# Optimization experiments

Measured on AMD Instinct MI355X. Metric: run time of the kernel, lower is better.

The kernel has to match this reference:

```python
import math
import jax, jax.numpy as jnp
from jax import lax
import numpy as np

BSZ, NQ, L, DM, DI, H, HD, DDIST, DCONV, DHID = 2, 128, 2048, 256, 512, 8, 64, 16, 4, 64
DKEY = DI * 2 + 2 + H  # key_proj output: z + xbc + per-head dt bias
DCV = DI + 2           # depthwise conv channels


def setup_inputs() -> dict:
    key = jax.random.key(0)
    ks = jax.random.split(key, 40)
    it = iter(range(40))
    def n(shape, s=1.0):
        return jax.random.normal(ks[next(it)], shape, jnp.float32) * s
    # dt_bias init exactly as in torch module
    dt = jnp.exp(jax.random.uniform(ks[next(it)], (H,)) * (math.log(0.1) - math.log(0.001)) + math.log(0.001))
    dt = jnp.maximum(dt, 1e-4)
    dt_bias = dt + jnp.log(-jnp.expm1(-dt))
    A_log = jnp.log(jax.random.uniform(ks[next(it)], (H,), minval=1.0, maxval=16.0))
    return {
        'queries': n((BSZ, NQ, DM)), 'anchors': n((BSZ, NQ, 3), 10.0),
        'features_perm': n((BSZ, L, DM)), 'pos_embed_perm': n((BSZ, L, DM)),
        'key_pos_3d': n((BSZ, L, 3), 10.0), 'query_pos': n((BSZ, NQ, DM)),
        'key_proj_w': n((DM, DKEY), 0.02),
        'key_conv_w': n((DCV, DCONV), 0.1), 'key_conv_b': jnp.zeros((DCV,)),
        'query_proj_w': n((DM, DI), 0.02),
        'dist_w1': n((3, DHID), 0.3), 'dist_b1': jnp.zeros((DHID,)), 'dist_w2': n((DHID, DDIST), 0.1),
        'bc_proj_w': n((DDIST, 2), 0.2), 'dt_proj_w': n((DDIST, H), 0.2),
        'dt_bias': dt_bias, 'A_log': A_log, 'D': jnp.ones((H,)),
        'key_norm_w': jnp.ones((DI,)), 'out_key_proj_w': n((DI, DM), 0.02),
        'query_norm_w': jnp.ones((DI,)), 'query_norm_b': jnp.zeros((DI,)),
        'out_query_proj_w': n((DI, DM), 0.02),
        'ffn_norm_w': jnp.ones((DM,)), 'ffn_norm_b': jnp.zeros((DM,)),
        'ffn_fc1_w': n((DM, 8 * DM), 0.02), 'ffn_fc1_b': jnp.zeros((8 * DM,)),
        'ffn_fc2_w': n((4 * DM, DM), 0.02), 'ffn_fc2_b': jnp.zeros((DM,)),
    }


def _ln(x, w, b, eps=1e-5):
    m = jnp.mean(x, -1, keepdims=True)
    v = jnp.mean((x - m) ** 2, -1, keepdims=True)
    return (x - m) * lax.rsqrt(v + eps) * w + b


def _dwconv_causal(x, w, b):
    # x [B,L,C], w [C,K]; torch pads K-1 both sides then slices [:L] == causal left pad
    lhs = jnp.swapaxes(x, 1, 2)  # [B,C,L]
    out = lax.conv_general_dilated(lhs, w[:, None, :], (1,), [(DCONV - 1, 0)],
                                   feature_group_count=w.shape[0],
                                   dimension_numbers=('NCH', 'OIH', 'NCH'))
    return jnp.swapaxes(out + b[None, :, None], 1, 2)


def _issm(x, dt, A, Bs, Cs, Dp, init):
    # x [B,L,H,P]; dt [B,L,H,N]; A [H,N]; Bs/Cs [B,L,N]; init [B,H,P,N]
    def step(h, inp):
        xt, dtt, bt, ct = inp  # [B,H,P], [B,H,N], [B,N], [B,N]
        h = h * jnp.exp(dtt * A)[:, :, None, :] + (dtt * bt[:, None, :])[:, :, None, :] * xt[..., None]
        return h, jnp.einsum('bhpn,bn->bhp', h, ct)
    xs = (jnp.swapaxes(x, 0, 1), jnp.swapaxes(dt, 0, 1), jnp.swapaxes(Bs, 0, 1), jnp.swapaxes(Cs, 0, 1))
    h_last, ys = lax.scan(step, init, xs)
    y = jnp.swapaxes(ys, 0, 1) + x * Dp[None, None, :, None]  # D skip inside scan, as in ISSM_chunk_scan_combined
    return y, h_last


def _forward(queries, anchors, features_perm, pos_embed_perm, key_pos_3d, query_pos,
             key_proj_w, key_conv_w, key_conv_b, query_proj_w, dist_w1, dist_b1, dist_w2,
             bc_proj_w, dt_proj_w, dt_bias, A_log, D, key_norm_w, out_key_proj_w,
             query_norm_w, query_norm_b, out_query_proj_w, ffn_norm_w, ffn_norm_b,
             ffn_fc1_w, ffn_fc1_b, ffn_fc2_w, ffn_fc2_b):
    qp = queries + query_pos
    kp = (features_perm + pos_embed_perm) @ key_proj_w            # [B,L,DKEY]
    z, xbc, dtb_seq = kp[..., :DI], kp[..., DI:DI + DCV], kp[..., DI + DCV:]
    xbc = jax.nn.silu(_dwconv_causal(xbc, key_conv_w, key_conv_b))
    x = xbc[..., :DI]
    b_bias, c_bias = xbc[..., DI], xbc[..., DI + 1]               # [B,L]
    init = (qp @ query_proj_w).reshape(BSZ, NQ, H, HD).transpose(0, 2, 3, 1)  # [B,H,HD,NQ]
    # distance features: delta [B,L,NQ,3]
    delta = anchors[:, None, :, :] - key_pos_3d[:, :, None, :]
    enc = jnp.sign(delta) * jnp.log2(jnp.abs(delta) * 20.0 + 1.0) / math.log2(8.0) / 4.0
    feat = jax.nn.relu(enc @ dist_w1 + dist_b1) @ dist_w2         # [B,L,NQ,DDIST]
    bc = feat @ bc_proj_w                                         # [B,L,NQ,2]
    Bssm = bc[..., 0] + b_bias[..., None]                         # [B,L,NQ]
    Cssm = bc[..., 1] + c_bias[..., None]
    dtb = jnp.swapaxes(feat @ dt_proj_w, 2, 3)                    # [B,L,H,NQ]
    dt = jax.nn.softplus(dtb + dtb_seq[..., None] + dt_bias[None, None, :, None])
    A = jnp.broadcast_to(-jnp.exp(A_log)[:, None], (H, NQ))
    xs = x.reshape(BSZ, L, H, HD)
    y_f, h_f = _issm(xs, dt, A, Bssm, Cssm, D, init)
    fl = lambda a: jnp.flip(a, axis=1)
    y_b, h_b = _issm(fl(xs), fl(dt), A, fl(Bssm), fl(Cssm), D, init)
    y = (y_f + fl(y_b)) * 0.5
    h = (h_f + h_b) * 0.5                                         # [B,H,HD,NQ]
    y = y.reshape(BSZ, L, DI) + x * jnp.repeat(D, HD)[None, None, :]
    # gated RMSNorm (norm_before_gate=False): gate first, then normalize
    g = y * jax.nn.silu(z)
    g = g * lax.rsqrt(jnp.mean(g * g, -1, keepdims=True) + 1e-5) * key_norm_w
    out_feat = features_perm + g @ out_key_proj_w
    hs = h.transpose(0, 3, 1, 2).reshape(BSZ, NQ, DI)             # b h hd n -> b n (h hd)
    out_q = queries + _ln(hs, query_norm_w, query_norm_b) @ out_query_proj_w
    fn = _ln(out_q, ffn_norm_w, ffn_norm_b)
    a, v = jnp.split(fn @ ffn_fc1_w + ffn_fc1_b, 2, axis=-1)
    out_q = out_q + (jax.nn.gelu(a, approximate=False) * v) @ ffn_fc2_w + ffn_fc2_b
    return out_q, out_feat


def reference(queries, anchors, features_perm, pos_embed_perm, key_pos_3d, query_pos,
              key_proj_w, key_conv_w, key_conv_b, query_proj_w, dist_w1, dist_b1, dist_w2,
              bc_proj_w, dt_proj_w, dt_bias, A_log, D, key_norm_w, out_key_proj_w,
              query_norm_w, query_norm_b, out_query_proj_w, ffn_norm_w, ffn_norm_b,
              ffn_fc1_w, ffn_fc1_b, ffn_fc2_w, ffn_fc2_b):
    return _forward(queries, anchors, features_perm, pos_embed_perm, key_pos_3d, query_pos,
                    key_proj_w, key_conv_w, key_conv_b, query_proj_w, dist_w1, dist_b1, dist_w2,
                    bc_proj_w, dt_proj_w, dt_bias, A_log, D, key_norm_w, out_key_proj_w,
                    query_norm_w, query_norm_b, out_query_proj_w, ffn_norm_w, ffn_norm_b,
                    ffn_fc1_w, ffn_fc1_b, ffn_fc2_w, ffn_fc2_b)
```

## Files before the change

### kernel.cpp

```cpp
#include <hip/hip_runtime.h>

typedef unsigned short u16;
typedef __bf16 bf16x8 __attribute__((ext_vector_type(8)));
typedef u16 u16x8 __attribute__((ext_vector_type(8)));
typedef float f32x4 __attribute__((ext_vector_type(4)));
typedef float f32x2 __attribute__((ext_vector_type(2)));

#define BSZ_ 2
#define NQ_ 128
#define LSEQ_ 2048
#define DM_ 256
#define DI_ 512
#define NH_ 8
#define HD_ 64
#define DKEY_ 1034
#define DCV_ 514
#define NCHUNK_ 16
#define CT_ 128

__device__ __forceinline__ float bf2f(u16 u) {
  unsigned v = ((unsigned)u) << 16;
  return __builtin_bit_cast(float, v);
}
__device__ __forceinline__ u16 f2bf(float f) {
  unsigned u = __builtin_bit_cast(unsigned, f);
  u += 0x7fffu + ((u >> 16) & 1u);
  return (u16)(u >> 16);
}
__device__ __forceinline__ float sigmoidf_(float x) { return 1.f / (1.f + expf(-x)); }
__device__ __forceinline__ float softplusf_(float x) {
  return (x > 20.f) ? x : log1pf(expf(x));
}

template<bool F32>
__device__ __forceinline__ float ldi(const void* p, size_t i) {
  return F32 ? ((const float*)p)[i] : bf2f(((const u16*)p)[i]);
}
template<bool F32>
__device__ __forceinline__ void sto(void* p, size_t i, float v) {
  if (F32) ((float*)p)[i] = v;
  else ((u16*)p)[i] = f2bf(v);
}

__device__ __forceinline__ bool detect_f32(const void* feat) {
  int lane = threadIdx.x & 63;
  float a = fabsf(bf2f(((const u16*)feat)[2*lane]));
  bool plaus = (a > 1e-6f) && (a < 1e6f);
  unsigned long long m = __ballot(plaus);
  return __popcll(m) < 32;
}

constexpr size_t SZ_KP    = (size_t)BSZ_*LSEQ_*DKEY_;
constexpr size_t SZ_XACT  = (size_t)BSZ_*LSEQ_*DCV_;
constexpr size_t SZ_AW    = (size_t)BSZ_*NH_*LSEQ_*NQ_*2;
constexpr size_t SZ_CARR  = (size_t)BSZ_*LSEQ_*NQ_;
constexpr size_t SZ_QPROJ = (size_t)BSZ_*NQ_*DI_;
constexpr size_t SZ_YACC  = (size_t)BSZ_*LSEQ_*DI_;
constexpr size_t SZ_SEND  = (size_t)BSZ_*NH_*2*NCHUNK_*NQ_*HD_;
constexpr size_t SZ_PTOT  = (size_t)BSZ_*NH_*2*NCHUNK_*NQ_;
constexpr size_t SZ_H0    = SZ_SEND;
constexpr size_t SZ_HB    = (size_t)BSZ_*NH_*2*NQ_*HD_;
constexpr size_t SZ_GBUF  = (size_t)BSZ_*LSEQ_*DI_/2;
constexpr size_t SZ_OUTQF = (size_t)BSZ_*NQ_*DM_;
constexpr size_t SZ_WPREP = 2048;

constexpr size_t OFF_KP    = 0;
constexpr size_t OFF_XACT  = OFF_KP + SZ_KP;
constexpr size_t OFF_AW    = OFF_XACT + SZ_XACT;
constexpr size_t OFF_CARR  = OFF_AW + SZ_AW;
constexpr size_t OFF_QPROJ = OFF_CARR + SZ_CARR;
constexpr size_t OFF_YACC  = OFF_QPROJ + SZ_QPROJ;
constexpr size_t OFF_SEND  = OFF_YACC + SZ_YACC;
constexpr size_t OFF_PTOT  = OFF_SEND + SZ_SEND;
constexpr size_t OFF_H0    = OFF_PTOT + SZ_PTOT;
constexpr size_t OFF_HB    = OFF_H0 + SZ_H0;
constexpr size_t OFF_GBUF  = OFF_HB + SZ_HB;
constexpr size_t OFF_OUTQF = OFF_GBUF + SZ_GBUF;
constexpr size_t OFF_WPREP = OFF_OUTQF + SZ_OUTQF;
constexpr size_t WS_FLOATS = OFF_WPREP + SZ_WPREP;

constexpr size_t OFF_UG  = OFF_AW;
constexpr size_t OFF_LNQ = OFF_UG + (size_t)256*1024/2;
constexpr size_t OFF_LNF = OFF_LNQ + (size_t)256*512/2;

constexpr size_t OFF_ABUF = OFF_SEND;
constexpr size_t OFF_AQ   = OFF_ABUF + (size_t)4096*256/2;
constexpr size_t OFF_BKEY = OFF_AQ + (size_t)256*256/2;
constexpr size_t OFF_BQ   = OFF_BKEY + (size_t)(256*1034+1)/2 + 1;
constexpr size_t OFF_BOK  = OFF_SEND;
constexpr size_t OFF_BOQ  = OFF_BOK + (size_t)512*256/2;
constexpr size_t OFF_B1W  = OFF_BOQ + (size_t)512*256/2;
constexpr size_t OFF_B2W  = OFF_B1W + (size_t)256*2048/2;

template<bool F32>
__device__ void prep_body(const void* A_log, const void* dt_bias,
                          const void* w1, const void* b1, const void* w2,
                          const void* bcw, const void* dtw, float* wp) {
  int t = threadIdx.x;
  if (t < 8) {
    wp[t]     = -expf(ldi<F32>(A_log, t));
    wp[8 + t] = ldi<F32>(dt_bias, t);
  }
  if (t < 64) {
    wp[32 + t*4 + 0] = ldi<F32>(w1, 0*64 + t);
    wp[32 + t*4 + 1] = ldi<F32>(w1, 1*64 + t);
    wp[32 + t*4 + 2] = ldi<F32>(w1, 2*64 + t);
    wp[32 + t*4 + 3] = ldi<F32>(b1, t);
  }
  for (int i = t; i < 1024; i += 256) wp[288 + i] = ldi<F32>(w2, i);
  if (t < 32)  wp[1312 + t] = ldi<F32>(bcw, t);
  if (t < 128) wp[1344 + t] = ldi<F32>(dtw, t);
}

__device__ __forceinline__ void cast_job(bool F32, const void* s0, const void* s1_,
                                         u16* d, size_t n, size_t base, size_t stride) {
  for (size_t i = base; i < n; i += stride) {
    float v = F32 ? ((const float*)s0)[i] : bf2f(((const u16*)s0)[i]);
    if (s1_) v += F32 ? ((const float*)s1_)[i] : bf2f(((const u16*)s1_)[i]);
    d[i] = f2bf(v);
  }
}

__global__ __launch_bounds__(256) void setup_kernel(
    const void* feat, const void* pe, u16* abuf,
    const void* q, const void* qp, u16* aq,
    const void* kw, u16* bkey, const void* qw, u16* bq,
    const void* A_log, const void* dt_bias, const void* w1, const void* b1,
    const void* w2, const void* bcw, const void* dtw, float* wp,
    float* yacc, int* flag)
{
  int bx = blockIdx.x, tid = threadIdx.x;
  if (bx < 512) {
    size_t base = (size_t)bx * 4096 + tid;
#pragma unroll
    for (int k = 0; k < 16; ++k) yacc[base + (size_t)k*256] = 0.f;
    return;
  }
  bool F32 = detect_f32(feat);
  if (bx < 1024) {
    cast_job(F32, feat, pe, abuf, (size_t)4096*256,
             (size_t)(bx-512)*256 + tid, (size_t)512*256);
  } else if (bx < 1056) {
    cast_job(F32, q, qp, aq, (size_t)256*256,
             (size_t)(bx-1024)*256 + tid, (size_t)32*256);
  } else if (bx < 1184) {
    cast_job(F32, kw, nullptr, bkey, (size_t)256*1034,
             (size_t)(bx-1056)*256 + tid, (size_t)128*256);
  } else if (bx < 1248) {
    cast_job(F32, qw, nullptr, bq, (size_t)256*512,
             (size_t)(bx-1184)*256 + tid, (size_t)64*256);
  } else {
    if (tid == 0) *flag = F32 ? 1 : 0;
    if (F32) prep_body<true>(A_log, dt_bias, w1, b1, w2, bcw, dtw, wp);
    else     prep_body<false>(A_log, dt_bias, w1, b1, w2, bcw, dtw, wp);
  }
}

template<int A_MODE, int B_MODE, int OUT_EXT, int RES_EXT, int RES_F32, int BIAS, bool F32>
__device__ void gemm_body(int bm, int bn,
                          const void* A0, const void* A1, const void* Bw,
                          float* Cf, void* Cext, const void* ResE,
                          const float* ResF, const void* Bias,
                          int M, int N, int K) {
  __shared__ u16 As[64][40];
  __shared__ u16 Bs[64][42];
  int tid = threadIdx.x;
  int w = tid >> 6, lane = tid & 63;
  f32x4 acc[4];
#pragma unroll
  for (int j = 0; j < 4; ++j) acc[j] = (f32x4){0.f, 0.f, 0.f, 0.f};

  int arow = tid >> 2, aseg = (tid & 3) * 8;
  int bkl = tid >> 3, bns = (tid & 7) * 8;

  for (int k0 = 0; k0 < K; k0 += 32) {
    {
      size_t abase = (size_t)(bm + arow) * K + k0 + aseg;
      u16x8 tv;
      if (A_MODE == 0) {
#pragma unroll
        for (int i = 0; i < 8; ++i)
          tv[i] = f2bf(ldi<F32>(A0, abase + i) + ldi<F32>(A1, abase + i));
      } else {
        const u16* pa = (const u16*)A0 + abase;
#pragma unroll
        for (int i = 0; i < 8; ++i) tv[i] = pa[i];
      }
      *(u16x8*)&As[arow][aseg] = tv;
    }
    {
      size_t bbase = (size_t)(k0 + bkl) * N + bn + bns;
#pragma unroll
      for (int i = 0; i < 8; ++i) {
        u16 v;
        if (bn + bns + i < N) {
          if (B_MODE == 1) v = ((const u16*)Bw)[bbase + i];
          else             v = f2bf(ldi<F32>(Bw, bbase + i));
        } else v = (u16)0;
        Bs[bns + i][bkl] = v;
      }
    }
    __syncthreads();
    int mrow = w * 16 + (lane & 15);
    int kq = (lane >> 4) * 8;
    bf16x8 af = __builtin_bit_cast(bf16x8, *(const u16x8*)&As[mrow][kq]);
#pragma unroll
    for (int j = 0; j < 4; ++j) {
      bf16x8 bfv = __builtin_bit_cast(bf16x8, *(const u16x8*)&Bs[j*16 + (lane & 15)][kq]);
      acc[j] = __builtin_amdgcn_mfma_f32_16x16x32_bf16(af, bfv, acc[j], 0, 0, 0);
    }
    __syncthreads();
  }
  int col0 = lane & 15, rbase = (lane >> 4) * 4;
#pragma unroll
  for (int j = 0; j < 4; ++j) {
#pragma unroll
    for (int r = 0; r < 4; ++r) {
      int row = bm + w * 16 + rbase + r;
      int col = bn + j * 16 + col0;
      if (col < N) {
        size_t idx = (size_t)row * N + col;
        float v = acc[j][r];
        if (BIAS)    v += ldi<F32>(Bias, col);
        if (RES_EXT) v += ldi<F32>(ResE, idx);
        if (RES_F32) v += ResF[idx];
        if (OUT_EXT) sto<F32>(Cext, idx, v);
        else         Cf[idx] = v;
      }
    }
  }
}

__global__ __launch_bounds__(256) void kp_gemm_kernel(
    const u16* abuf, const u16* bkey, float* kp) {
  gemm_body<1,1,0,0,0,0,false>(blockIdx.x*64, blockIdx.y*64, abuf, nullptr, bkey,
                               kp, nullptr, nullptr, nullptr, nullptr,
                               4096, DKEY_, DM_);
}

template<bool F32>
__device__ void fc2_body(const u16* ug, const u16* b2w, void* out_q,
                         const float* outqf, const void* b2) {
  gemm_body<1,1,1,0,1,1,F32>((blockIdx.x&3)*64, (blockIdx.x>>2)*64, ug, nullptr,
                             b2w, nullptr, out_q, nullptr, outqf, b2,
                             BSZ_*NQ_, DM_, 1024);
}
__global__ __launch_bounds__(256) void fc2_kernel(
    const int* fl, const u16* ug, const u16* b2w, void* out_q,
    const float* outqf, const void* b2) {
  if (*fl) fc2_body<true>(ug, b2w, out_q, outqf, b2);
  else     fc2_body<false>(ug, b2w, out_q, outqf, b2);
}

template<bool F32>
__device__ void conv_body(const float* kp, const void* cw, const void* cb,
                          float* xact) {
  int row = blockIdx.x;
  int l = row & (LSEQ_ - 1);
  for (int ch = threadIdx.x; ch < DCV_; ch += 256) {
    float acc = ldi<F32>(cb, ch);
#pragma unroll
    for (int k = 0; k < 4; ++k) {
      int ll = l - 3 + k;
      if (ll >= 0)
        acc = fmaf(ldi<F32>(cw, ch*4 + k), kp[(size_t)(row - 3 + k)*DKEY_ + DI_ + ch], acc);
    }
    xact[(size_t)row*DCV_ + ch] = acc * sigmoidf_(acc);
  }
}
__global__ __launch_bounds__(256) void convqp_kernel(
    const int* fl, const float* kp, const void* cw, const void* cb, float* xact,
    const u16* aq, const u16* bq, float* qproj)
{
  int bx = blockIdx.x;
  if (bx < 4096) {
    if (*fl) conv_body<true>(kp, cw, cb, xact);
    else     conv_body<false>(kp, cw, cb, xact);
  } else {
    int i = bx - 4096;
    gemm_body<1,1,0,0,0,0,false>((i&3)*64, (i>>2)*64, aq, nullptr, bq,
                                 qproj, nullptr, nullptr, nullptr, nullptr,
                                 BSZ_*NQ_, DI_, DM_);
  }
}

template<bool F32>
__device__ void dist_body(const void* anchors, const void* key_pos,
                          const float* kp, const float* xact, const float* wp,
                          float* aw, float* carr) {
  int tid = threadIdx.x;
  int n = tid & 127;
  int idx = blockIdx.x;
  int b = idx >> 10;
  int l = ((idx & 1023) << 1) | (tid >> 7);
  size_t row = (size_t)b * LSEQ_ + l;

  float enc0, enc1, enc2;
  {
    float e[3];
#pragma unroll
    for (int d = 0; d < 3; ++d) {
      float delta = ldi<F32>(anchors, (b*NQ_ + n)*3 + d) - ldi<F32>(key_pos, row*3 + d);
      float s = delta < 0.f ? -1.f : 1.f;
      e[d] = s * log2f(fabsf(delta) * 20.f + 1.f) * (1.f/12.f);
    }
    enc0 = e[0]; enc1 = e[1]; enc2 = e[2];
  }
  float feat[16];
#pragma unroll
  for (int f = 0; f < 16; ++f) feat[f] = 0.f;
  for (int j = 0; j < 64; ++j) {
    float w0 = wp[32 + j*4], w1v = wp[33 + j*4], w2v = wp[34 + j*4], bb = wp[35 + j*4];
    float hj = fmaxf(fmaf(enc0, w0, fmaf(enc1, w1v, fmaf(enc2, w2v, bb))), 0.f);
#pragma unroll
    for (int f = 0; f < 16; ++f) feat[f] = fmaf(hj, wp[288 + j*16 + f], feat[f]);
  }
  float bc0 = 0.f, bc1 = 0.f;
#pragma unroll
  for (int f = 0; f < 16; ++f) {
    bc0 = fmaf(feat[f], wp[1312 + f*2], bc0);
    bc1 = fmaf(feat[f], wp[1313 + f*2], bc1);
  }
  float bb_ = xact[row*DCV_ + DI_];
  float cb_ = xact[row*DCV_ + DI_ + 1];
  float Bs = bc0 + bb_, Cs = bc1 + cb_;
  carr[row*NQ_ + n] = Cs;

  float dtb[8];
#pragma unroll
  for (int h = 0; h < 8; ++h) dtb[h] = 0.f;
#pragma unroll
  for (int f = 0; f < 16; ++f)
#pragma unroll
    for (int h = 0; h < 8; ++h) dtb[h] = fmaf(feat[f], wp[1344 + f*8 + h], dtb[h]);

#pragma unroll
  for (int h = 0; h < 8; ++h) {
    float xln = dtb[h] + kp[row*DKEY_ + (DI_*2 + 2) + h] + wp[8 + h];
    float dtv = softplusf_(xln);
    float a = expf(dtv * wp[h]);
    float wv = dtv * Bs;
    size_t o = (((size_t)(b*NH_ + h)*LSEQ_ + l)*NQ_ + n)*2;
    aw[o] = a;
    aw[o + 1] = wv;
  }
}
__global__ __launch_bounds__(256) void dist_kernel(
    const int* fl, const void* anchors, const void* key_pos, const float* kp,
    const float* xact, const float* wp, float* aw, float* carr) {
  if (*fl) dist_body<true>(anchors, key_pos, kp, xact, wp, aw, carr);
  else     dist_body<false>(anchors, key_pos, kp, xact, wp, aw, carr);
}

__global__ __launch_bounds__(256) void s1m_kernel(
    const float* __restrict__ aw, const float* __restrict__ xact,
    float* __restrict__ send, float* __restrict__ ptot)
{
  __shared__ float awl[2][8][32];
  __shared__ float xl [2][8][64];
  int tid = threadIdx.x;
  int hd = tid & 63;
  int w = __builtin_amdgcn_readfirstlane(tid >> 6);
  int ns = blockIdx.x, q = blockIdx.y, z = blockIdx.z;
  int h = z & 7, b = z >> 3;
  int n0 = __builtin_amdgcn_readfirstlane(ns*16 + w*4);

  float hf[4], hb[4], pr[4];
#pragma unroll
  for (int i = 0; i < 4; ++i) { hf[i] = 0.f; hb[i] = 0.f; pr[i] = 1.f; }

  int s8 = tid >> 5, j = tid & 31;
  int t0 = q*CT_;
  const float* awg = aw + (size_t)z*LSEQ_*(NQ_*2)
                     + (size_t)(t0 + s8)*(NQ_*2) + ns*32 + j;
  const float* xg  = xact + ((size_t)(b*LSEQ_) + t0 + s8)*DCV_ + (h<<6) + j*2;
  const long awgstep = 8L*(NQ_*2);
  const long xgstep  = 8L*DCV_;

  {
    float pa = *awg;
    f32x2 px = *(const f32x2*)xg;
    awg += awgstep; xg += xgstep;
    awl[0][s8][j] = pa;
    *(f32x2*)&xl[0][s8][j*2] = px;
  }
  asm volatile("s_waitcnt lgkmcnt(0)" ::: "memory");
  __builtin_amdgcn_s_barrier();

  int p = 0;
  float sa; f32x2 sx;
  for (int g = 0; g < 16; ++g) {
    if (g < 15) {
      sa = *awg; sx = *(const f32x2*)xg;
      awg += awgstep; xg += xgstep;
    }
#pragma unroll
    for (int s = 0; s < 8; ++s) {
      const float* A = &awl[p][s][w*8];
      float xv = xl[p][s][hd];
#pragma unroll
      for (int i = 0; i < 4; ++i) {
        float a = A[2*i], wv = A[2*i + 1];
        float wx = wv * xv;
        hf[i] = fmaf(hf[i], a, wx);
        hb[i] = fmaf(pr[i], wx, hb[i]);
        pr[i] *= a;
      }
    }
    if (g < 15) {
      awl[p^1][s8][j] = sa;
      *(f32x2*)&xl[p^1][s8][j*2] = sx;
    }
    asm volatile("s_waitcnt lgkmcnt(0)" ::: "memory");
    __builtin_amdgcn_s_barrier();
    p ^= 1;
  }

  size_t cbf = (size_t)((z*2 + 0)*NCHUNK_ + q);
  size_t cbb = (size_t)((z*2 + 1)*NCHUNK_ + (NCHUNK_ - 1 - q));
#pragma unroll
  for (int i = 0; i < 4; ++i) {
    send[cbf*(NQ_*HD_) + (size_t)(n0 + i)*HD_ + hd] = hf[i];
    send[cbb*(NQ_*HD_) + (size_t)(n0 + i)*HD_ + hd] = hb[i];
  }
  if (hd == 0) {
#pragma unroll
    for (int i = 0; i < 4; ++i) {
      ptot[cbf*NQ_ + n0 + i] = pr[i];
      ptot[cbb*NQ_ + n0 + i] = pr[i];
    }
  }
}

__global__ __launch_bounds__(256) void s2_kernel(
    const float* __restrict__ qproj, const float* __restrict__ ptot,
    const float* __restrict__ send, float* __restrict__ h0buf,
    float* __restrict__ hbuf)
{
  int g = blockIdx.x*256 + threadIdx.x;
  int hd = g & 63;
  int n = (g >> 6) & 127;
  int dir = (g >> 13) & 1;
  int h = (g >> 14) & 7;
  int b = g >> 17;
  float hcur = qproj[((size_t)(b*NQ_ + n))*DI_ + h*HD_ + hd];
  size_t base = (size_t)((b*NH_ + h)*2 + dir) * NCHUNK_;
  for (int q = 0; q < NCHUNK_; ++q) {
    size_t cb = base + q;
    h0buf[cb*(NQ_*HD_) + (size_t)n*HD_ + hd] = hcur;
    hcur = fmaf(hcur, ptot[cb*NQ_ + n], send[cb*(NQ_*HD_) + (size_t)n*HD_ + hd]);
  }
  hbuf[((size_t)((b*NH_ + h)*2 + dir))*(NQ_*HD_) + (size_t)n*HD_ + hd] = hcur;
}

template<bool F32>
__device__ void cast1_part(const void* okw, u16* bok, const void* oqw, u16* boq,
                           const void* w1, u16* b1w, const void* w2, u16* b2w) {
  int i = blockIdx.x - 2048;
  int job = i >> 7, bj = i & 127;
  size_t base = (size_t)bj*256 + threadIdx.x, stride = (size_t)128*256;
  switch (job) {
    case 0: cast_job(F32, okw, nullptr, bok, (size_t)512*256, base, stride); break;
    case 1: cast_job(F32, oqw, nullptr, boq, (size_t)512*256, base, stride); break;
    case 2: cast_job(F32, w1, nullptr, b1w, (size_t)256*2048, base, stride); break;
    default: cast_job(F32, w2, nullptr, b2w, (size_t)1024*256, base, stride); break;
  }
}
__global__ __launch_bounds__(256) void s3cast_kernel(
    const int* fl, const float* __restrict__ aw, const float* __restrict__ carr,
    const float* __restrict__ xact, const float* __restrict__ h0buf,
    float* __restrict__ yacc,
    const void* okw, u16* bok, const void* oqw, u16* boq,
    const void* w1, u16* b1w, const void* w2, u16* b2w)
{
  int bx = blockIdx.x;
  if (bx >= 2048) {
    if (*fl) cast1_part<true>(okw, bok, oqw, boq, w1, b1w, w2, b2w);
    else     cast1_part<false>(okw, bok, oqw, boq, w1, b1w, w2, b2w);
    return;
  }
  __shared__ float awl[2][8][64];
  __shared__ float ctl[2][8][32];
  __shared__ float xl [2][8][64];
  __shared__ float yl [8][4][64];

  int tid = threadIdx.x;
  int hd = tid & 63;
  int w = __builtin_amdgcn_readfirstlane(tid >> 6);
  int ns = bx & 3, q = (bx >> 2) & 15, zz = bx >> 6;
  int dir = zz & 1, h = (zz >> 1) & 7, b = zz >> 4;
  int z = b*NH_ + h;
  int n0 = ns*32 + w*8;

  int tbase = dir ? (LSEQ_ - 1 - q*CT_) : (q*CT_);
  int tstep = dir ? -1 : 1;

  int s8 = tid >> 5, j = tid & 31;
  const float* awg = aw + (size_t)z*LSEQ_*(NQ_*2)
                     + (size_t)(tbase + tstep*s8)*(NQ_*2) + ns*64 + j*2;
  const float* ctg = carr + ((size_t)(b*LSEQ_) + tbase + tstep*s8)*NQ_ + ns*32 + j;
  const float* xg  = xact + ((size_t)(b*LSEQ_) + tbase + tstep*s8)*DCV_ + (h<<6) + j*2;
  long awgstep = (long)tstep*8*(NQ_*2);
  long ctgstep = (long)tstep*8*NQ_;
  long xgstep  = (long)tstep*8*DCV_;

  f32x2 pa = *(const f32x2*)awg;
  float pc = *ctg;
  f32x2 px = *(const f32x2*)xg;
  awg += awgstep; ctg += ctgstep; xg += xgstep;

  float h0_, h1_, h2_, h3_, h4_, h5_, h6_, h7_;
  {
    size_t cb = (size_t)((z*2 + dir)*NCHUNK_ + q);
    const float* hp = h0buf + cb*(NQ_*HD_) + (size_t)n0*HD_ + hd;
    h0_ = hp[0*HD_]; h1_ = hp[1*HD_]; h2_ = hp[2*HD_]; h3_ = hp[3*HD_];
    h4_ = hp[4*HD_]; h5_ = hp[5*HD_]; h6_ = hp[6*HD_]; h7_ = hp[7*HD_];
  }
  *(f32x2*)&awl[0][s8][j*2] = pa;
  ctl[0][s8][j] = pc;
  *(f32x2*)&xl[0][s8][j*2] = px;
  asm volatile("s_waitcnt lgkmcnt(0)" ::: "memory");
  __builtin_amdgcn_s_barrier();

  float* yrow = yacc + ((size_t)(b*LSEQ_) + tbase)*DI_ + (h << 6) + hd;
  long ystep = (long)tstep * DI_;

  int p = 0;
  f32x2 sa; float sc; f32x2 sx;
  for (int g = 0; g < 16; ++g) {
    if (g < 15) {
      sa = *(const f32x2*)awg; sc = *ctg; sx = *(const f32x2*)xg;
      awg += awgstep; ctg += ctgstep; xg += xgstep;
    }
    if (g > 0) {
#pragma unroll
      for (int r = 0; r < 2; ++r) {
        int s = w + r*4;
        float yv = yl[s][0][hd] + yl[s][1][hd] + yl[s][2][hd] + yl[s][3][hd];
        atomicAdd(yrow + (long)((g-1)*8 + s)*ystep, 0.5f * yv);
      }
    }
    asm volatile("s_waitcnt lgkmcnt(0)" ::: "memory");
    __builtin_amdgcn_s_barrier();
#pragma unroll
    for (int s = 0; s < 8; ++s) {
      const float* A = &awl[p][s][w*16];
      const float* C = &ctl[p][s][w*8];
      float xv = xl[p][s][hd];
      float ya, yb;
      h0_ = fmaf(h0_, A[0],  A[1]*xv);  ya = h0_ * C[0];
      h1_ = fmaf(h1_, A[2],  A[3]*xv);  yb = h1_ * C[1];
      h2_ = fmaf(h2_, A[4],  A[5]*xv);  ya = fmaf(h2_, C[2], ya);
      h3_ = fmaf(h3_, A[6],  A[7]*xv);  yb = fmaf(h3_, C[3], yb);
      h4_ = fmaf(h4_, A[8],  A[9]*xv);  ya = fmaf(h4_, C[4], ya);
      h5_ = fmaf(h5_, A[10], A[11]*xv); yb = fmaf(h5_, C[5], yb);
      h6_ = fmaf(h6_, A[12], A[13]*xv); ya = fmaf(h6_, C[6], ya);
      h7_ = fmaf(h7_, A[14], A[15]*xv); yb = fmaf(h7_, C[7], yb);
      yl[s][w][hd] = ya + yb;
    }
    if (g < 15) {
      *(f32x2*)&awl[p^1][s8][j*2] = sa;
      ctl[p^1][s8][j] = sc;
      *(f32x2*)&xl[p^1][s8][j*2] = sx;
    }
    asm volatile("s_waitcnt lgkmcnt(0)" ::: "memory");
    __builtin_amdgcn_s_barrier();
    p ^= 1;
  }
#pragma unroll
  for (int r = 0; r < 2; ++r) {
    int s = w + r*4;
    float yv = yl[s][0][hd] + yl[s][1][hd] + yl[s][2][hd] + yl[s][3][hd];
    atomicAdd(yrow + (long)(15*8 + s)*ystep, 0.5f * yv);
  }
}

__device__ __forceinline__ float block_sum256(float v, float* red) {
#pragma unroll
  for (int off = 32; off; off >>= 1) v += __shfl_xor(v, off, 64);
  int wv = threadIdx.x >> 6;
  if ((threadIdx.x & 63) == 0) red[wv] = v;
  __syncthreads();
  float t = red[0] + red[1] + red[2] + red[3];
  __syncthreads();
  return t;
}

template<bool F32>
__device__ void g_body(const float* yacc, const float* xact, const float* kp,
                       const void* Dv, const void* knw, u16* gbuf) {
  int row = blockIdx.x, tid = threadIdx.x;
  __shared__ float red[4];
  float gg[2];
  float ss = 0.f;
#pragma unroll
  for (int ii = 0; ii < 2; ++ii) {
    int ch = tid + ii*256;
    float yv = yacc[(size_t)row*DI_ + ch];
    float xv = xact[(size_t)row*DCV_ + ch];
    float zv = kp[(size_t)row*DKEY_ + ch];
    float Dh = ldi<F32>(Dv, ch >> 6);
    float yf = yv + 2.f * Dh * xv;
    float g = yf * (zv * sigmoidf_(zv));
    gg[ii] = g;
    ss += g * g;
  }
  float tot = block_sum256(ss, red);
  float r = rsqrtf(tot / (float)DI_ + 1e-5f);
#pragma unroll
  for (int ii = 0; ii < 2; ++ii) {
    int ch = tid + ii*256;
    gbuf[(size_t)row*DI_ + ch] = f2bf(gg[ii] * r * ldi<F32>(knw, ch));
  }
}
template<bool F32>
__device__ void lnq_body(const float* hbuf, const void* qnw, const void* qnb,
                         u16* lnq) {
  int row = blockIdx.x - 4096;
  int b = row >> 7, n = row & 127;
  int tid = threadIdx.x;
  __shared__ float red[4];
  float hv[2];
  float s1 = 0.f, s2 = 0.f;
#pragma unroll
  for (int ii = 0; ii < 2; ++ii) {
    int ch = tid + ii*256;
    int h = ch >> 6, hd = ch & 63;
    size_t base = ((size_t)((b*NH_ + h)*2))*(NQ_*HD_) + (size_t)n*HD_ + hd;
    float v = 0.5f * (hbuf[base] + hbuf[base + (size_t)NQ_*HD_]);
    hv[ii] = v;
    s1 += v;
    s2 += v * v;
  }
  s1 = block_sum256(s1, red);
  s2 = block_sum256(s2, red);
  float mean = s1 / (float)DI_;
  float var = fmaxf(s2 / (float)DI_ - mean * mean, 0.f);
  float rstd = rsqrtf(var + 1e-5f);
#pragma unroll
  for (int ii = 0; ii < 2; ++ii) {
    int ch = tid + ii*256;
    lnq[(size_t)row*DI_ + ch] =
        f2bf((hv[ii] - mean) * rstd * ldi<F32>(qnw, ch) + ldi<F32>(qnb, ch));
  }
}
__global__ __launch_bounds__(256) void glnq_kernel(
    const int* fl, const float* yacc, const float* xact, const float* kp,
    const void* Dv, const void* knw, u16* gbuf,
    const float* hbuf, const void* qnw, const void* qnb, u16* lnq)
{
  if (blockIdx.x < 4096) {
    if (*fl) g_body<true>(yacc, xact, kp, Dv, knw, gbuf);
    else     g_body<false>(yacc, xact, kp, Dv, knw, gbuf);
  } else {
    if (*fl) lnq_body<true>(hbuf, qnw, qnb, lnq);
    else     lnq_body<false>(hbuf, qnw, qnb, lnq);
  }
}

template<bool F32>
__device__ void ofoq_body(const u16* gbuf, const u16* bok, void* out_feat,
                          const void* features, const u16* lnq, const u16* boq,
                          float* outqf, const void* queries) {
  int bx = blockIdx.x;
  if (bx < 256) {
    gemm_body<1,1,1,1,0,0,F32>((bx>>2)*64, (bx&3)*64, gbuf, nullptr, bok,
                               nullptr, out_feat, features, nullptr, nullptr,
                               4096, DM_, DI_);
  } else {
    int i = bx - 256;
    gemm_body<1,1,0,1,0,0,F32>((i&3)*64, (i>>2)*64, lnq, nullptr, boq,
                               outqf, nullptr, queries, nullptr, nullptr,
                               BSZ_*NQ_, DM_, DI_);
  }
}
__global__ __launch_bounds__(256) void ofoq_kernel(
    const int* fl, const u16* gbuf, const u16* bok,
    void* out_feat_f32, void* out_feat_bf16, const void* features,
    const u16* lnq, const u16* boq, float* outqf, const void* queries) {
  if (*fl) ofoq_body<true>(gbuf, bok, out_feat_f32, features, lnq, boq, outqf, queries);
  else     ofoq_body<false>(gbuf, bok, out_feat_bf16, features, lnq, boq, outqf, queries);
}

template<bool F32>
__device__ void lnf_body(const float* outqf, const void* fnw, const void* fnb,
                         u16* lnf) {
  int row = blockIdx.x, tid = threadIdx.x;
  __shared__ float red[4];
  float x = outqf[(size_t)row*DM_ + tid];
  float s1 = block_sum256(x, red);
  float s2 = block_sum256(x * x, red);
  float mean = s1 / (float)DM_;
  float var = fmaxf(s2 / (float)DM_ - mean * mean, 0.f);
  float rstd = rsqrtf(var + 1e-5f);
  lnf[(size_t)row*DM_ + tid] =
      f2bf((x - mean) * rstd * ldi<F32>(fnw, tid) + ldi<F32>(fnb, tid));
}
__global__ __launch_bounds__(256) void lnf_kernel(
    const int* fl, const float* outqf, const void* fnw, const void* fnb, u16* lnf) {
  if (*fl) lnf_body<true>(outqf, fnw, fnb, lnf);
  else     lnf_body<false>(outqf, fnw, fnb, lnf);
}

template<bool F32>
__device__ void fc1g_body(const u16* lnf, const u16* b1w, const void* b1, u16* ug) {
  __shared__ u16 As[64][40];
  __shared__ u16 BsA[64][42];
  __shared__ u16 BsV[64][42];
  int tid = threadIdx.x;
  int w = tid >> 6, lane = tid & 63;
  int bm = blockIdx.x * 64, bn = blockIdx.y * 64;
  f32x4 accA[4], accV[4];
#pragma unroll
  for (int j = 0; j < 4; ++j) {
    accA[j] = (f32x4){0.f, 0.f, 0.f, 0.f};
    accV[j] = (f32x4){0.f, 0.f, 0.f, 0.f};
  }
  int arow = tid >> 2, aseg = (tid & 3) * 8;
  int bkl = tid >> 3, bns = (tid & 7) * 8;

  for (int k0 = 0; k0 < DM_; k0 += 32) {
    {
      size_t abase = (size_t)(bm + arow) * DM_ + k0 + aseg;
      const u16* pa = lnf + abase;
      u16x8 tv;
#pragma unroll
      for (int i = 0; i < 8; ++i) tv[i] = pa[i];
      *(u16x8*)&As[arow][aseg] = tv;
    }
    {
      size_t bbase = (size_t)(k0 + bkl) * 2048 + bn + bns;
#pragma unroll
      for (int i = 0; i < 8; ++i) {
        BsA[bns + i][bkl] = b1w[bbase + i];
        BsV[bns + i][bkl] = b1w[bbase + 1024 + i];
      }
    }
    __syncthreads();
    int mrow = w * 16 + (lane & 15);
    int kq = (lane >> 4) * 8;
    bf16x8 af = __builtin_bit_cast(bf16x8, *(const u16x8*)&As[mrow][kq]);
#pragma unroll
    for (int j = 0; j < 4; ++j) {
      bf16x8 ba = __builtin_bit_cast(bf16x8, *(const u16x8*)&BsA[j*16 + (lane & 15)][kq]);
      bf16x8 bv = __builtin_bit_cast(bf16x8, *(const u16x8*)&BsV[j*16 + (lane & 15)][kq]);
      accA[j] = __builtin_amdgcn_mfma_f32_16x16x32_bf16(af, ba, accA[j], 0, 0, 0);
      accV[j] = __builtin_amdgcn_mfma_f32_16x16x32_bf16(af, bv, accV[j], 0, 0, 0);
    }
    __syncthreads();
  }
  int col0 = lane & 15, rbase = (lane >> 4) * 4;
#pragma unroll
  for (int j = 0; j < 4; ++j) {
#pragma unroll
    for (int r = 0; r < 4; ++r) {
      int row = bm + w * 16 + rbase + r;
      int col = bn + j * 16 + col0;
      float a = accA[j][r] + ldi<F32>(b1, col);
      float v = accV[j][r] + ldi<F32>(b1, col + 1024);
      float ge = 0.5f * a * (1.f + erff(a * 0.70710678118f));
      ug[(size_t)row*1024 + col] = f2bf(ge * v);
    }
  }
}
__global__ __launch_bounds__(256) void fc1g_kernel(
    const int* fl, const u16* lnf, const u16* b1w, const void* b1, u16* ug) {
  if (*fl) fc1g_body<true>(lnf, b1w, b1, ug);
  else     fc1g_body<false>(lnf, b1w, b1, ug);
}

extern "C" void kernel_launch(void* const* d_in, const int* in_sizes, int n_in,
                              void* d_out, int out_size, void* d_ws, size_t ws_size,
                              hipStream_t stream) {
  const void* queries        = d_in[0];
  const void* anchors        = d_in[1];
  const void* features       = d_in[2];
  const void* pos_embed      = d_in[3];
  const void* key_pos        = d_in[4];
  const void* query_pos      = d_in[5];
  const void* key_proj_w     = d_in[6];
  const void* key_conv_w     = d_in[7];
  const void* key_conv_b     = d_in[8];
  const void* query_proj_w   = d_in[9];
  const void* dist_w1        = d_in[10];
  const void* dist_b1        = d_in[11];
  const void* dist_w2        = d_in[12];
  const void* bc_proj_w      = d_in[13];
  const void* dt_proj_w      = d_in[14];
  const void* dt_bias        = d_in[15];
  const void* A_log          = d_in[16];
  const void* Dvec           = d_in[17];
  const void* key_norm_w     = d_in[18];
  const void* out_key_proj_w = d_in[19];
  const void* query_norm_w   = d_in[20];
  const void* query_norm_b   = d_in[21];
  const void* out_query_proj_w = d_in[22];
  const void* ffn_norm_w     = d_in[23];
  const void* ffn_norm_b     = d_in[24];
  const void* ffn_fc1_w      = d_in[25];
  const void* ffn_fc1_b      = d_in[26];
  const void* ffn_fc2_w      = d_in[27];
  const void* ffn_fc2_b      = d_in[28];

  if (ws_size < WS_FLOATS * sizeof(float)) return;

  float* ws    = (float*)d_ws;
  float* kp    = ws + OFF_KP;
  float* xact  = ws + OFF_XACT;
  float* aw    = ws + OFF_AW;
  float* carr  = ws + OFF_CARR;
  float* qproj = ws + OFF_QPROJ;
  float* yacc  = ws + OFF_YACC;
  float* send  = ws + OFF_SEND;
  float* ptot  = ws + OFF_PTOT;
  float* h0buf = ws + OFF_H0;
  float* hbuf  = ws + OFF_HB;
  u16*   gbuf  = (u16*)(ws + OFF_GBUF);
  float* outqf = ws + OFF_OUTQF;
  float* wprep = ws + OFF_WPREP;
  int*   flag  = (int*)(wprep + 1536);
  u16*   ugbuf = (u16*)(ws + OFF_UG);
  u16*   lnq   = (u16*)(ws + OFF_LNQ);
  u16*   lnf   = (u16*)(ws + OFF_LNF);
  u16*   abuf  = (u16*)(ws + OFF_ABUF);
  u16*   aq    = (u16*)(ws + OFF_AQ);
  u16*   bkey  = (u16*)(ws + OFF_BKEY);
  u16*   bq    = (u16*)(ws + OFF_BQ);
  u16*   bok   = (u16*)(ws + OFF_BOK);
  u16*   boq   = (u16*)(ws + OFF_BOQ);
  u16*   b1w   = (u16*)(ws + OFF_B1W);
  u16*   b2w   = (u16*)(ws + OFF_B2W);

  void* out_q = d_out;
  void* out_feat_bf16 = (void*)((u16*)d_out + (size_t)BSZ_*NQ_*DM_);
  void* out_feat_f32  = (void*)((float*)d_out + (size_t)BSZ_*NQ_*DM_);

  setup_kernel<<<1249, 256, 0, stream>>>(
      features, pos_embed, abuf, queries, query_pos, aq,
      key_proj_w, bkey, query_proj_w, bq,
      A_log, dt_bias, dist_w1, dist_b1, dist_w2, bc_proj_w, dt_proj_w, wprep,
      yacc, flag);

  kp_gemm_kernel<<<dim3(64, 17), 256, 0, stream>>>(abuf, bkey, kp);

  convqp_kernel<<<4096 + 32, 256, 0, stream>>>(
      flag, kp, key_conv_w, key_conv_b, xact, aq, bq, qproj);

  dist_kernel<<<BSZ_*LSEQ_/2, 256, 0, stream>>>(flag, anchors, key_pos, kp, xact,
                                                wprep, aw, carr);

  s1m_kernel<<<dim3(8, NCHUNK_, BSZ_*NH_), 256, 0, stream>>>(aw, xact, send, ptot);

  s2_kernel<<<1024, 256, 0, stream>>>(qproj, ptot, send, h0buf, hbuf);

  s3cast_kernel<<<2048 + 512, 256, 0, stream>>>(
      flag, aw, carr, xact, h0buf, yacc,
      out_key_proj_w, bok, out_query_proj_w, boq, ffn_fc1_w, b1w, ffn_fc2_w, b2w);

  glnq_kernel<<<4096 + 256, 256, 0, stream>>>(
      flag, yacc, xact, kp, Dvec, key_norm_w, gbuf,
      hbuf, query_norm_w, query_norm_b, lnq);

  ofoq_kernel<<<256 + 16, 256, 0, stream>>>(
      flag, gbuf, bok, out_feat_f32, out_feat_bf16, features,
      lnq, boq, outqf, queries);

  lnf_kernel<<<BSZ_*NQ_, 256, 0, stream>>>(flag, outqf, ffn_norm_w, ffn_norm_b, lnf);

  fc1g_kernel<<<dim3(4, 16), 256, 0, stream>>>(flag, lnf, b1w, ffn_fc1_b, ugbuf);

  fc2_kernel<<<16, 256, 0, stream>>>(flag, ugbuf, b2w, out_q, outqf, ffn_fc2_b);
}
```

Measured before the change: 423.0 us.

## Fuse conv/dist/qproj launches, fold FFN LayerNorm into fc1, vectorize GEMM loads

New measurement: 437.8 us. +3.5%, slower.

```diff
diff --git a/kernel.cpp b/kernel.cpp
--- a/kernel.cpp
+++ b/kernel.cpp
@@ -3,6 +3,7 @@
 typedef unsigned short u16;
 typedef __bf16 bf16x8 __attribute__((ext_vector_type(8)));
 typedef u16 u16x8 __attribute__((ext_vector_type(8)));
+typedef u16 u16x2 __attribute__((ext_vector_type(2)));
 typedef float f32x4 __attribute__((ext_vector_type(4)));
 typedef float f32x2 __attribute__((ext_vector_type(2)));
 
@@ -81,7 +82,6 @@
 
 constexpr size_t OFF_UG  = OFF_AW;
 constexpr size_t OFF_LNQ = OFF_UG + (size_t)256*1024/2;
-constexpr size_t OFF_LNF = OFF_LNQ + (size_t)256*512/2;
 
 constexpr size_t OFF_ABUF = OFF_SEND;
 constexpr size_t OFF_AQ   = OFF_ABUF + (size_t)4096*256/2;
@@ -156,7 +156,7 @@
   }
 }
 
-template<int A_MODE, int B_MODE, int OUT_EXT, int RES_EXT, int RES_F32, int BIAS, bool F32>
+template<int A_MODE, int B_MODE, int BV, int OUT_EXT, int RES_EXT, int RES_F32, int BIAS, bool F32>
 __device__ void gemm_body(int bm, int bn,
                           const void* A0, const void* A1, const void* Bw,
                           float* Cf, void* Cext, const void* ResE,
@@ -182,22 +182,34 @@
         for (int i = 0; i < 8; ++i)
           tv[i] = f2bf(ldi<F32>(A0, abase + i) + ldi<F32>(A1, abase + i));
       } else {
-        const u16* pa = (const u16*)A0 + abase;
-#pragma unroll
-        for (int i = 0; i < 8; ++i) tv[i] = pa[i];
+        tv = *(const u16x8*)((const u16*)A0 + abase);
       }
       *(u16x8*)&As[arow][aseg] = tv;
     }
     {
       size_t bbase = (size_t)(k0 + bkl) * N + bn + bns;
-#pragma unroll
-      for (int i = 0; i < 8; ++i) {
-        u16 v;
-        if (bn + bns + i < N) {
-          if (B_MODE == 1) v = ((const u16*)Bw)[bbase + i];
-          else             v = f2bf(ldi<F32>(Bw, bbase + i));
-        } else v = (u16)0;
-        Bs[bns + i][bkl] = v;
+      if (BV == 2) {
+        u16x8 bv8 = *(const u16x8*)((const u16*)Bw + bbase);
+#pragma unroll
+        for (int i = 0; i < 8; ++i) Bs[bns + i][bkl] = bv8[i];
+      } else if (BV == 1 && bn + bns + 8 <= N) {
+        const u16* bp = (const u16*)Bw + bbase;
+#pragma unroll
+        for (int i2 = 0; i2 < 4; ++i2) {
+          u16x2 v2 = *(const u16x2*)(bp + i2*2);
+          Bs[bns + i2*2][bkl]     = v2[0];
+          Bs[bns + i2*2 + 1][bkl] = v2[1];
+        }
+      } else {
+#pragma unroll
+        for (int i = 0; i < 8; ++i) {
+          u16 v;
+          if (bn + bns + i < N) {
+            if (B_MODE == 1) v = ((const u16*)Bw)[bbase + i];
+            else             v = f2bf(ldi<F32>(Bw, bbase + i));
+          } else v = (u16)0;
+          Bs[bns + i][bkl] = v;
+        }
       }
     }
     __syncthreads();
@@ -233,17 +245,17 @@
 
 __global__ __launch_bounds__(256) void kp_gemm_kernel(
     const u16* abuf, const u16* bkey, float* kp) {
-  gemm_body<1,1,0,0,0,0,false>(blockIdx.x*64, blockIdx.y*64, abuf, nullptr, bkey,
-                               kp, nullptr, nullptr, nullptr, nullptr,
-                               4096, DKEY_, DM_);
+  gemm_body<1,1,1,0,0,0,0,false>(blockIdx.x*64, blockIdx.y*64, abuf, nullptr, bkey,
+                                 kp, nullptr, nullptr, nullptr, nullptr,
+                                 4096, DKEY_, DM_);
 }
 
 template<bool F32>
 __device__ void fc2_body(const u16* ug, const u16* b2w, void* out_q,
                          const float* outqf, const void* b2) {
-  gemm_body<1,1,1,0,1,1,F32>((blockIdx.x&3)*64, (blockIdx.x>>2)*64, ug, nullptr,
-                             b2w, nullptr, out_q, nullptr, outqf, b2,
-                             BSZ_*NQ_, DM_, 1024);
+  gemm_body<1,1,2,1,0,1,1,F32>((blockIdx.x&3)*64, (blockIdx.x>>2)*64, ug, nullptr,
+                               b2w, nullptr, out_q, nullptr, outqf, b2,
+                               BSZ_*NQ_, DM_, 1024);
 }
 __global__ __launch_bounds__(256) void fc2_kernel(
     const int* fl, const u16* ug, const u16* b2w, void* out_q,
@@ -254,8 +266,7 @@
 
 template<bool F32>
 __device__ void conv_body(const float* kp, const void* cw, const void* cb,
-                          float* xact) {
-  int row = blockIdx.x;
+                          float* xact, int row) {
   int l = row & (LSEQ_ - 1);
   for (int ch = threadIdx.x; ch < DCV_; ch += 256) {
     float acc = ldi<F32>(cb, ch);
@@ -268,26 +279,11 @@
     xact[(size_t)row*DCV_ + ch] = acc * sigmoidf_(acc);
   }
 }
-__global__ __launch_bounds__(256) void convqp_kernel(
-    const int* fl, const float* kp, const void* cw, const void* cb, float* xact,
-    const u16* aq, const u16* bq, float* qproj)
-{
-  int bx = blockIdx.x;
-  if (bx < 4096) {
-    if (*fl) conv_body<true>(kp, cw, cb, xact);
-    else     conv_body<false>(kp, cw, cb, xact);
-  } else {
-    int i = bx - 4096;
-    gemm_body<1,1,0,0,0,0,false>((i&3)*64, (i>>2)*64, aq, nullptr, bq,
-                                 qproj, nullptr, nullptr, nullptr, nullptr,
-                                 BSZ_*NQ_, DI_, DM_);
-  }
-}
 
 template<bool F32>
 __device__ void dist_body(const void* anchors, const void* key_pos,
-                          const float* kp, const float* xact, const float* wp,
-                          float* aw, float* carr) {
+                          const float* kp, const void* cw, const void* cb,
+                          const float* wp, float* aw, float* carr) {
   int tid = threadIdx.x;
   int n = tid & 127;
   int idx = blockIdx.x;
@@ -306,6 +302,19 @@
     }
     enc0 = e[0]; enc1 = e[1]; enc2 = e[2];
   }
+  float acc0 = ldi<F32>(cb, 512);
+  float acc1 = ldi<F32>(cb, 513);
+#pragma unroll
+  for (int k = 0; k < 4; ++k) {
+    int ll = l - 3 + k;
+    if (ll >= 0) {
+      acc0 = fmaf(ldi<F32>(cw, 512*4 + k), kp[(row - 3 + k)*DKEY_ + DI_ + 512], acc0);
+      acc1 = fmaf(ldi<F32>(cw, 513*4 + k), kp[(row - 3 + k)*DKEY_ + DI_ + 513], acc1);
+    }
+  }
+  float bb_ = acc0 * sigmoidf_(acc0);
+  float cb_ = acc1 * sigmoidf_(acc1);
+
   float feat[16];
 #pragma unroll
   for (int f = 0; f < 16; ++f) feat[f] = 0.f;
@@ -321,8 +330,6 @@
     bc0 = fmaf(feat[f], wp[1312 + f*2], bc0);
     bc1 = fmaf(feat[f], wp[1313 + f*2], bc1);
   }
-  float bb_ = xact[row*DCV_ + DI_];
-  float cb_ = xact[row*DCV_ + DI_ + 1];
   float Bs = bc0 + bb_, Cs = bc1 + cb_;
   carr[row*NQ_ + n] = Cs;
 
@@ -345,11 +352,26 @@
     aw[o + 1] = wv;
   }
 }
-__global__ __launch_bounds__(256) void dist_kernel(
-    const int* fl, const void* anchors, const void* key_pos, const float* kp,
-    const float* xact, const float* wp, float* aw, float* carr) {
-  if (*fl) dist_body<true>(anchors, key_pos, kp, xact, wp, aw, carr);
-  else     dist_body<false>(anchors, key_pos, kp, xact, wp, aw, carr);
+
+__global__ __launch_bounds__(256) void cdq_kernel(
+    const int* fl, const float* kp, const void* cw, const void* cb, float* xact,
+    const u16* aq, const u16* bq, float* qproj,
+    const void* anchors, const void* key_pos, const float* wp,
+    float* aw, float* carr)
+{
+  int bx = blockIdx.x;
+  if (bx < 2048) {
+    if (*fl) dist_body<true>(anchors, key_pos, kp, cw, cb, wp, aw, carr);
+    else     dist_body<false>(anchors, key_pos, kp, cw, cb, wp, aw, carr);
+  } else if (bx < 6144) {
+    if (*fl) conv_body<true>(kp, cw, cb, xact, bx - 2048);
+    else     conv_body<false>(kp, cw, cb, xact, bx - 2048);
+  } else {
+    int i = bx - 6144;
+    gemm_body<1,1,2,0,0,0,0,false>((i&3)*64, (i>>2)*64, aq, nullptr, bq,
+                                   qproj, nullptr, nullptr, nullptr, nullptr,
+                                   BSZ_*NQ_, DI_, DM_);
+  }
 }
 
 __global__ __launch_bounds__(256) void s1m_kernel(
@@ -664,14 +686,14 @@
                           float* outqf, const void* queries) {
   int bx = blockIdx.x;
   if (bx < 256) {
-    gemm_body<1,1,1,1,0,0,F32>((bx>>2)*64, (bx&3)*64, gbuf, nullptr, bok,
-                               nullptr, out_feat, features, nullptr, nullptr,
-                               4096, DM_, DI_);
+    gemm_body<1,1,2,1,1,0,0,F32>((bx>>2)*64, (bx&3)*64, gbuf, nullptr, bok,
+                                 nullptr, out_feat, features, nullptr, nullptr,
+                                 4096, DM_, DI_);
   } else {
     int i = bx - 256;
-    gemm_body<1,1,0,1,0,0,F32>((i&3)*64, (i>>2)*64, lnq, nullptr, boq,
-                               outqf, nullptr, queries, nullptr, nullptr,
-                               BSZ_*NQ_, DM_, DI_);
+    gemm_body<1,1,2,0,1,0,0,F32>((i&3)*64, (i>>2)*64, lnq, nullptr, boq,
+                                 outqf, nullptr, queries, nullptr, nullptr,
+                                 BSZ_*NQ_, DM_, DI_);
   }
 }
 __global__ __launch_bounds__(256) void ofoq_kernel(
@@ -683,63 +705,63 @@
 }
 
 template<bool F32>
-__device__ void lnf_body(const float* outqf, const void* fnw, const void* fnb,
-                         u16* lnf) {
-  int row = blockIdx.x, tid = threadIdx.x;
-  __shared__ float red[4];
-  float x = outqf[(size_t)row*DM_ + tid];
-  float s1 = block_sum256(x, red);
-  float s2 = block_sum256(x * x, red);
-  float mean = s1 / (float)DM_;
-  float var = fmaxf(s2 / (float)DM_ - mean * mean, 0.f);
-  float rstd = rsqrtf(var + 1e-5f);
-  lnf[(size_t)row*DM_ + tid] =
-      f2bf((x - mean) * rstd * ldi<F32>(fnw, tid) + ldi<F32>(fnb, tid));
-}
-__global__ __launch_bounds__(256) void lnf_kernel(
-    const int* fl, const float* outqf, const void* fnw, const void* fnb, u16* lnf) {
-  if (*fl) lnf_body<true>(outqf, fnw, fnb, lnf);
-  else     lnf_body<false>(outqf, fnw, fnb, lnf);
-}
-
-template<bool F32>
-__device__ void fc1g_body(const u16* lnf, const u16* b1w, const void* b1, u16* ug) {
-  __shared__ u16 As[64][40];
+__device__ void fc1g_body(const float* outqf, const void* fnw, const void* fnb,
+                          const u16* b1w, const void* b1, u16* ug) {
+  __shared__ u16 Asf[64][264];
   __shared__ u16 BsA[64][42];
   __shared__ u16 BsV[64][42];
+  __shared__ float red1[64][4];
+  __shared__ float red2[64][4];
   int tid = threadIdx.x;
   int w = tid >> 6, lane = tid & 63;
   int bm = blockIdx.x * 64, bn = blockIdx.y * 64;
+
+  {
+    int r = tid >> 2, qt = tid & 3;
+    const float* src = outqf + (size_t)(bm + r)*DM_ + qt*64;
+    float v[64];
+    float s1 = 0.f, s2 = 0.f;
+#pragma unroll
+    for (int i = 0; i < 64; ++i) { v[i] = src[i]; s1 += v[i]; s2 += v[i]*v[i]; }
+    red1[r][qt] = s1; red2[r][qt] = s2;
+    __syncthreads();
+    float t1 = red1[r][0] + red1[r][1] + red1[r][2] + red1[r][3];
+    float t2 = red2[r][0] + red2[r][1] + red2[r][2] + red2[r][3];
+    float mean = t1 / (float)DM_;
+    float var = fmaxf(t2 / (float)DM_ - mean * mean, 0.f);
+    float rstd = rsqrtf(var + 1e-5f);
+#pragma unroll
+    for (int i = 0; i < 64; ++i) {
+      int col = qt*64 + i;
+      Asf[r][col] = f2bf((v[i] - mean) * rstd * ldi<F32>(fnw, col)
+                         + ldi<F32>(fnb, col));
+    }
+    __syncthreads();
+  }
+
   f32x4 accA[4], accV[4];
 #pragma unroll
   for (int j = 0; j < 4; ++j) {
     accA[j] = (f32x4){0.f, 0.f, 0.f, 0.f};
     accV[j] = (f32x4){0.f, 0.f, 0.f, 0.f};
   }
-  int arow = tid >> 2, aseg = (tid & 3) * 8;
   int bkl = tid >> 3, bns = (tid & 7) * 8;
 
   for (int k0 = 0; k0 < DM_; k0 += 32) {
     {
-      size_t abase = (size_t)(bm + arow) * DM_ + k0 + aseg;
-      const u16* pa = lnf + abase;
-      u16x8 tv;
-#pragma unroll
-      for (int i = 0; i < 8; ++i) tv[i] = pa[i];
-      *(u16x8*)&As[arow][aseg] = tv;
-    }
-    {
       size_t bbase = (size_t)(k0 + bkl) * 2048 + bn + bns;
+      u16x8 ba8 = *(const u16x8*)(b1w + bbase);
+      u16x8 bv8 = *(const u16x8*)(b1w + bbase + 1024);
 #pragma unroll
       for (int i = 0; i < 8; ++i) {
-        BsA[bns + i][bkl] = b1w[bbase + i];
-        BsV[bns + i][bkl] = b1w[bbase + 1024 + i];
+        BsA[bns + i][bkl] = ba8[i];
+        BsV[bns + i][bkl] = bv8[i];
       }
     }
     __syncthreads();
     int mrow = w * 16 + (lane & 15);
     int kq = (lane >> 4) * 8;
-    bf16x8 af = __builtin_bit_cast(bf16x8, *(const u16x8*)&As[mrow][kq]);
+    bf16x8 af = __builtin_bit_cast(bf16x8, *(const u16x8*)&Asf[mrow][k0 + kq]);
 #pragma unroll
     for (int j = 0; j < 4; ++j) {
       bf16x8 ba = __builtin_bit_cast(bf16x8, *(const u16x8*)&BsA[j*16 + (lane & 15)][kq]);
@@ -764,9 +786,10 @@
   }
 }
 __global__ __launch_bounds__(256) void fc1g_kernel(
-    const int* fl, const u16* lnf, const u16* b1w, const void* b1, u16* ug) {
-  if (*fl) fc1g_body<true>(lnf, b1w, b1, ug);
-  else     fc1g_body<false>(lnf, b1w, b1, ug);
+    const int* fl, const float* outqf, const void* fnw, const void* fnb,
+    const u16* b1w, const void* b1, u16* ug) {
+  if (*fl) fc1g_body<true>(outqf, fnw, fnb, b1w, b1, ug);
+  else     fc1g_body<false>(outqf, fnw, fnb, b1w, b1, ug);
 }
 
 extern "C" void kernel_launch(void* const* d_in, const int* in_sizes, int n_in,
@@ -821,7 +844,6 @@
   int*   flag  = (int*)(wprep + 1536);
   u16*   ugbuf = (u16*)(ws + OFF_UG);
   u16*   lnq   = (u16*)(ws + OFF_LNQ);
-  u16*   lnf   = (u16*)(ws + OFF_LNF);
   u16*   abuf  = (u16*)(ws + OFF_ABUF);
   u16*   aq    = (u16*)(ws + OFF_AQ);
   u16*   bkey  = (u16*)(ws + OFF_BKEY);
@@ -843,11 +865,9 @@
 
   kp_gemm_kernel<<<dim3(64, 17), 256, 0, stream>>>(abuf, bkey, kp);
 
-  convqp_kernel<<<4096 + 32, 256, 0, stream>>>(
-      flag, kp, key_conv_w, key_conv_b, xact, aq, bq, qproj);
-
-  dist_kernel<<<BSZ_*LSEQ_/2, 256, 0, stream>>>(flag, anchors, key_pos, kp, xact,
-                                                wprep, aw, carr);
+  cdq_kernel<<<2048 + 4096 + 32, 256, 0, stream>>>(
+      flag, kp, key_conv_w, key_conv_b, xact, aq, bq, qproj,
+      anchors, key_pos, wprep, aw, carr);
 
   s1m_kernel<<<dim3(8, NCHUNK_, BSZ_*NH_), 256, 0, stream>>>(aw, xact, send, ptot);
 
@@ -865,9 +885,8 @@
       flag, gbuf, bok, out_feat_f32, out_feat_bf16, features,
       lnq, boq, outqf, queries);
 
-  lnf_kernel<<<BSZ_*NQ_, 256, 0, stream>>>(flag, outqf, ffn_norm_w, ffn_norm_b, lnf);
-
-  fc1g_kernel<<<dim3(4, 16), 256, 0, stream>>>(flag, lnf, b1w, ffn_fc1_b, ugbuf);
+  fc1g_kernel<<<dim3(4, 16), 256, 0, stream>>>(
+      flag, outqf, ffn_norm_w, ffn_norm_b, b1w, ffn_fc1_b, ugbuf);
 
   fc2_kernel<<<16, 256, 0, stream>>>(flag, ugbuf, b2w, out_q, outqf, ffn_fc2_b);
 }
```
